# Kernel optimization log

Measured on AMD Instinct MI355X. Metric: run time of the kernel, lower is better.

The kernel has to match this reference:

```python
import jax, jax.numpy as jnp
import numpy as np
import math

P = 2
TAU = 1.0
USE_POW = False
ALIGN_W = 1.0
ENTROPY_W = 1.0
EPS = 1e-12


def _pairwise_l2(z):
    # torch.cdist(z, z, p=2): sqrt of squared distances via GEMM decomposition
    sq = jnp.sum(z * z, axis=-1)  # [N]
    d2 = sq[:, None] + sq[None, :] - 2.0 * (z @ z.T)  # [N, N]
    d = jnp.sqrt(jnp.maximum(d2, 0.0))
    return jnp.maximum(d, EPS)  # clamp_min(eps)


def setup_inputs() -> dict:
    key = jax.random.key(0)
    k0, k1 = jax.random.split(key)
    v0 = jax.random.normal(k0, (8192, 256), dtype=jnp.float32)
    v1 = jax.random.normal(k1, (8192, 256), dtype=jnp.float32)
    return {"v0": v0, "v1": v1}


def reference(v0, v1):
    views = [v0, v1]
    n = v0.shape[0]

    # Alignment term: mean Lp distance between matched rows, one pair (0,1)
    diff = v0 - v1
    align = jnp.sqrt(jnp.sum(diff * diff, axis=-1)).mean()  # p=2 norm per row

    # Entropy term: masked logsumexp over within-view pairwise distances
    log_num_neg = math.log(n - 1)
    eye = jnp.eye(n, dtype=bool)
    entropy = jnp.float32(0.0)
    for z in views:
        dist = _pairwise_l2(z)  # [N, N]
        logits = jnp.where(eye, -jnp.inf, -dist / TAU)
        lme = jax.nn.logsumexp(logits, axis=1) - log_num_neg  # [N]
        entropy = entropy + lme.mean()
    entropy = entropy / len(views)

    return ALIGN_W * align + ENTROPY_W * entropy
```

## Files before the change

### kernel.cpp

```cpp
#include <hip/hip_runtime.h>
#include <math.h>


#define D_DIM 256
#define NB 64
#define NSEG 1056
#define S_Q 26.0f
#define LOG2E2 2.0813689810f
#define LP 65

typedef int i32x4 __attribute__((ext_vector_type(4)));
typedef unsigned int u32;
#define AS1 __attribute__((address_space(1)))
#define AS3 __attribute__((address_space(3)))

__device__ inline void load_lds16(const void* g, void* l) {
  __builtin_amdgcn_global_load_lds((const AS1 u32*)g, (AS3 u32*)l, 16, 0, 0);
}

__device__ inline int q8(float x) {
  return __float2int_rn(fminf(fmaxf(x * S_Q, -127.0f), 127.0f));
}
__device__ inline u32 q8x4(const float4 f) {
  return (u32)(q8(f.x) & 255) | ((u32)(q8(f.y) & 255) << 8) |
         ((u32)(q8(f.z) & 255) << 16) | ((u32)(q8(f.w) & 255) << 24);
}

__device__ inline int Gfun(int M) {
  const int m = M >> 1;
  return (M & 1) ? (m + 1) * (m + 1) : m * (m + 1);
}

__global__ __launch_bounds__(256) void prep(
    const float* __restrict__ v0, const float* __restrict__ v1,
    unsigned char* __restrict__ ph0, unsigned char* __restrict__ ph1,
    float* __restrict__ sq0, float* __restrict__ sq1,
    float* __restrict__ S0, float* __restrict__ S1,
    float* __restrict__ align_part) {
  __shared__ float4 l0[16 * LP], l1[16 * LP];
  __shared__ float red0[4][16], red1[4][16], red2[4][16];
  const int R = blockIdx.x;
  const int t = threadIdx.x;

  #pragma unroll
  for (int p = 0; p < 4; ++p) {
    const int slot = t + p * 256;
    const int r = slot >> 6, col = slot & 63;
    const size_t g = (size_t)(R * 16 + r) * 64 + col;
    l0[r * LP + col] = ((const float4*)v0)[g];
    l1[r * LP + col] = ((const float4*)v1)[g];
  }
  __syncthreads();

  {
    const int rr = t & 15, c = t >> 4;
    const int s = c >> 2, q = c & 3;
    const int li = rr * LP + c * 4;
    uint4 u0, u1;
    u0.x = q8x4(l0[li + 0]); u0.y = q8x4(l0[li + 1]);
    u0.z = q8x4(l0[li + 2]); u0.w = q8x4(l0[li + 3]);
    u1.x = q8x4(l1[li + 0]); u1.y = q8x4(l1[li + 1]);
    u1.z = q8x4(l1[li + 2]); u1.w = q8x4(l1[li + 3]);
    const size_t dst = (size_t)(R * 4 + s) * 64 + q * 16 + rr;
    ((uint4*)ph0)[dst] = u0;
    ((uint4*)ph1)[dst] = u1;
  }

  {
    const int rr = t & 15;
    const int base = rr * LP + (t >> 4) * 4;
    float s0p = 0.f, s1p = 0.f, s2p = 0.f;
    #pragma unroll
    for (int c = 0; c < 4; ++c) {
      const float4 a = l0[base + c], b = l1[base + c];
      s0p += a.x * a.x + a.y * a.y + a.z * a.z + a.w * a.w;
      s1p += b.x * b.x + b.y * b.y + b.z * b.z + b.w * b.w;
      const float dx = a.x - b.x, dy = a.y - b.y, dz = a.z - b.z, dw = a.w - b.w;
      s2p += dx * dx + dy * dy + dz * dz + dw * dw;
    }
    s0p += __shfl_xor(s0p, 16, 64); s0p += __shfl_xor(s0p, 32, 64);
    s1p += __shfl_xor(s1p, 16, 64); s1p += __shfl_xor(s1p, 32, 64);
    s2p += __shfl_xor(s2p, 16, 64); s2p += __shfl_xor(s2p, 32, 64);
    const int w = t >> 6, lane = t & 63;
    if (lane < 16) { red0[w][lane] = s0p; red1[w][lane] = s1p; red2[w][lane] = s2p; }
  }
  __syncthreads();
  if (t < 16) {
    const int row = R * 16 + t;
    const float a0 = red0[0][t] + red0[1][t] + red0[2][t] + red0[3][t];
    const float a1 = red1[0][t] + red1[1][t] + red1[2][t] + red1[3][t];
    const float a2 = red2[0][t] + red2[1][t] + red2[2][t] + red2[3][t];
    sq0[row] = a0 * LOG2E2;
    sq1[row] = a1 * LOG2E2;
    align_part[row] = sqrtf(a2);
    S0[row] = 0.0f;
    S1[row] = 0.0f;
  }
}

__global__ __launch_bounds__(256) void entropy_tile(
    const unsigned char* __restrict__ ph0, const unsigned char* __restrict__ ph1,
    const float* __restrict__ sq0, const float* __restrict__ sq1,
    float* __restrict__ S0, float* __restrict__ S1) {
  const unsigned char* __restrict__ ph = blockIdx.y ? ph1 : ph0;
  const float* __restrict__ sq = blockIdx.y ? sq1 : sq0;
  float* __restrict__ S        = blockIdx.y ? S1 : S0;

  const int lin = blockIdx.x;
  int bi = 0;
  while (NSEG - Gfun(64 - (bi + 1)) <= lin) ++bi;
  const int q = lin - (NSEG - Gfun(64 - bi));
  const int bj0 = bi + 2 * q;

  __shared__ __align__(16) char smem[32768];
  float* swp = (float*)smem;

  const int t = threadIdx.x, lane = t & 63, w = t >> 6;
  const int wi = w >> 1, wj = w & 1;
  const int quad = lane >> 4, l15 = lane & 15;
  const int i0 = bi * 128;

  #pragma unroll
  for (int r8 = 0; r8 < 8; ++r8) {
    const int seg = w * 8 + r8;
    const unsigned char* src = ph + (size_t)bi * 32768 + seg * 1024 + lane * 16;
    load_lds16(src, smem + seg * 1024);
  }
  __syncthreads();

  const i32x4* __restrict__ phv = (const i32x4*)ph;
  const i32x4* smemv = (const i32x4*)smem;
  const float K2 = 2.0f * LOG2E2 / (S_Q * S_Q);

  float prow[4][4];
  #pragma unroll
  for (int m = 0; m < 4; ++m)
    #pragma unroll
    for (int r = 0; r < 4; ++r) prow[m][r] = 0.f;

  auto do_tile = [&](const int bj, const bool diag_t) {
    const int j0 = bj * 128;
    const int baseB = ((bj * 8 + wj * 4) * 4) * 64 + lane;

    float sjl[4];
    #pragma unroll
    for (int n = 0; n < 4; ++n) sjl[n] = sq[j0 + wj * 64 + n * 16 + l15];

    i32x4 bF[4][4];
    #pragma unroll
    for (int s = 0; s < 4; ++s)
      #pragma unroll
      for (int n = 0; n < 4; ++n)
        bF[s][n] = phv[baseB + (n * 4 + s) * 64];

    float csum[4] = {0.f, 0.f, 0.f, 0.f};

    i32x4 accA[4], accB[4];
    float siA[4], siB[4];

    auto compute = [&](i32x4* acc, float* si, const int m) {
      #pragma unroll
      for (int r = 0; r < 4; ++r)
        si[r] = sq[i0 + wi * 64 + m * 16 + quad * 4 + r];
      #pragma unroll
      for (int n = 0; n < 4; ++n) acc[n] = (i32x4){0, 0, 0, 0};
      #pragma unroll
      for (int s = 0; s < 4; ++s) {
        const i32x4 ah = smemv[(size_t)((wi * 4 + m) * 4 + s) * 64 + lane];
        #pragma unroll
        for (int n = 0; n < 4; ++n)
          acc[n] = __builtin_amdgcn_mfma_i32_16x16x64_i8(ah, bF[s][n], acc[n], 0, 0, 0);
      }
    };

    auto epilogue = [&](const i32x4* acc, const float* si, const int m) {
      #pragma unroll
      for (int r = 0; r < 4; ++r) {
        const int gi = i0 + wi * 64 + m * 16 + quad * 4 + r;
        float p = 0.f;
        #pragma unroll
        for (int n = 0; n < 4; ++n) {
          const float d2 = fmaf(-K2, (float)acc[n][r], si[r] + sjl[n]);
          float e = __builtin_amdgcn_exp2f(-__builtin_amdgcn_sqrtf(d2));
          if (diag_t && gi == j0 + wj * 64 + n * 16 + l15) e = 0.f;
          p += e;
          csum[n] += e;
        }
        prow[m][r] += p;
      }
    };

    compute(accA, siA, 0);
    compute(accB, siB, 1);
    epilogue(accA, siA, 0);
    compute(accA, siA, 2);
    epilogue(accB, siB, 1);
    compute(accB, siB, 3);
    epilogue(accA, siA, 2);
    epilogue(accB, siB, 3);

    if (!diag_t) {
      #pragma unroll
      for (int n = 0; n < 4; ++n) {
        float c2 = csum[n];
        c2 += __shfl_xor(c2, 16, 64);
        c2 += __shfl_xor(c2, 32, 64);
        if (quad == 0) atomicAdd(&S[j0 + wj * 64 + n * 16 + l15], c2);
      }
    }
  };

  if (bj0 == bi) do_tile(bi, true); else do_tile(bj0, false);
  if (bj0 + 1 < NB) do_tile(bj0 + 1, false);

  __syncthreads();

  const int wbase = w * 1088;
  #pragma unroll
  for (int m = 0; m < 4; ++m)
    #pragma unroll
    for (int r = 0; r < 4; ++r)
      swp[wbase + (m * 16 + quad * 4 + r) * 17 + l15] = prow[m][r];
  float rs = 0.f;
  #pragma unroll
  for (int j = 0; j < 16; ++j) rs += swp[wbase + lane * 17 + j];
  atomicAdd(&S[i0 + wi * 64 + lane], rs);
}

__global__ __launch_bounds__(256) void finalize_part(
    const float* __restrict__ S0, const float* __restrict__ S1,
    const float* __restrict__ align_part,
    float* __restrict__ part_log, float* __restrict__ part_align) {
  __shared__ float shl[4], sha[4];
  const int t = threadIdx.x, lane = t & 63, w = t >> 6;
  const int idx = blockIdx.x * 256 + t;
  float lg = __logf(S0[idx]) + __logf(S1[idx]);
  float al = align_part[idx];
  #pragma unroll
  for (int o = 1; o < 64; o <<= 1) {
    lg += __shfl_xor(lg, o, 64);
    al += __shfl_xor(al, o, 64);
  }
  if (lane == 0) { shl[w] = lg; sha[w] = al; }
  __syncthreads();
  if (t == 0) {
    part_log[blockIdx.x] = shl[0] + shl[1] + shl[2] + shl[3];
    part_align[blockIdx.x] = sha[0] + sha[1] + sha[2] + sha[3];
  }
}

__global__ void finalize_final(const float* __restrict__ part_log,
                               const float* __restrict__ part_align,
                               float* __restrict__ out, int n) {
  const int lane = threadIdx.x & 63;
  double lg = (lane < 32) ? (double)part_log[lane] : 0.0;
  double al = (lane < 32) ? (double)part_align[lane] : 0.0;
  #pragma unroll
  for (int o = 1; o < 32; o <<= 1) {
    lg += __shfl_xor(lg, o, 64);
    al += __shfl_xor(al, o, 64);
  }
  if (lane == 0) {
    double align = al / (double)n;
    double entropy = 0.5 * lg / (double)n - log((double)(n - 1));
    out[0] = (float)(align + entropy);
  }
}

extern "C" void kernel_launch(void* const* d_in, const int* in_sizes, int n_in,
                              void* d_out, int out_size, void* d_ws, size_t ws_size,
                              hipStream_t stream) {
  const float* v0 = (const float*)d_in[0];
  const float* v1 = (const float*)d_in[1];
  float* out = (float*)d_out;
  const int n = in_sizes[0] / D_DIM;

  float* ws         = (float*)d_ws;
  float* sq0        = ws;
  float* sq1        = ws + n;
  float* S0         = ws + 2 * n;
  float* S1         = ws + 3 * n;
  float* align_part = ws + 4 * n;
  float* part_log   = ws + 5 * n;
  float* part_align = ws + 5 * n + 32;
  unsigned char* ph0 = (unsigned char*)(ws + 5 * n + 64);
  unsigned char* ph1 = ph0 + (size_t)n * D_DIM;

  prep<<<n / 16, 256, 0, stream>>>(v0, v1, ph0, ph1, sq0, sq1, S0, S1, align_part);

  dim3 grid(NSEG, 2);
  entropy_tile<<<grid, 256, 0, stream>>>(ph0, ph1, sq0, sq1, S0, S1);

  finalize_part<<<n / 256, 256, 0, stream>>>(S0, S1, align_part, part_log, part_align);
  finalize_final<<<1, 64, 0, stream>>>(part_log, part_align, out, n);
}
```

Baseline: 112.7 us.

## Prefetch next B tile during epilogue and fuse final reduction via atomic ticket

The entropy tile kernel now issues the global loads for the second column tile's B fragments and squared norms before the epilogue of the first tile runs, so their latency overlaps with exp/sqrt work. The first tile's B loads are also issued before the barrier that waits on the LDS fill. Separately, the two finalize kernels are merged into one, which accumulates partial sums with double atomics and lets the last block, chosen by an atomic ticket, write the output. This saves a kernel launch, but the accumulation order becomes nondeterministic and the prefetch keeps more registers live.

```diff
diff --git a/kernel.cpp b/kernel.cpp
--- a/kernel.cpp
+++ b/kernel.cpp
@@ -36,11 +36,14 @@
     unsigned char* __restrict__ ph0, unsigned char* __restrict__ ph1,
     float* __restrict__ sq0, float* __restrict__ sq1,
     float* __restrict__ S0, float* __restrict__ S1,
-    float* __restrict__ align_part) {
+    float* __restrict__ align_part,
+    double* __restrict__ totals, int* __restrict__ ticket) {
   __shared__ float4 l0[16 * LP], l1[16 * LP];
   __shared__ float red0[4][16], red1[4][16], red2[4][16];
   const int R = blockIdx.x;
   const int t = threadIdx.x;
+
+  if (R == 0 && t == 0) { totals[0] = 0.0; totals[1] = 0.0; ticket[0] = 0; }
 
   #pragma unroll
   for (int p = 0; p < 4; ++p) {
@@ -126,92 +129,112 @@
     const unsigned char* src = ph + (size_t)bi * 32768 + seg * 1024 + lane * 16;
     load_lds16(src, smem + seg * 1024);
   }
-  __syncthreads();
 
   const i32x4* __restrict__ phv = (const i32x4*)ph;
   const i32x4* smemv = (const i32x4*)smem;
   const float K2 = 2.0f * LOG2E2 / (S_Q * S_Q);
 
+  const int bjA = bj0;
+  const bool diagA = (bj0 == bi);
+  const bool haveB = (bj0 + 1 < NB);
+  const int j0A = bjA * 128;
+
   float prow[4][4];
   #pragma unroll
   for (int m = 0; m < 4; ++m)
     #pragma unroll
     for (int r = 0; r < 4; ++r) prow[m][r] = 0.f;
 
-  auto do_tile = [&](const int bj, const bool diag_t) {
-    const int j0 = bj * 128;
+  i32x4 bF[4][4];
+  float sjlA[4], sjlB[4];
+  float csumA[4] = {0.f, 0.f, 0.f, 0.f}, csumB[4] = {0.f, 0.f, 0.f, 0.f};
+  i32x4 accA[4], accB[4];
+  float siA[4], siB[4];
+
+  auto loadB = [&](const int bj) {
     const int baseB = ((bj * 8 + wj * 4) * 4) * 64 + lane;
-
-    float sjl[4];
-    #pragma unroll
-    for (int n = 0; n < 4; ++n) sjl[n] = sq[j0 + wj * 64 + n * 16 + l15];
-
-    i32x4 bF[4][4];
     #pragma unroll
     for (int s = 0; s < 4; ++s)
       #pragma unroll
       for (int n = 0; n < 4; ++n)
         bF[s][n] = phv[baseB + (n * 4 + s) * 64];
-
-    float csum[4] = {0.f, 0.f, 0.f, 0.f};
-
-    i32x4 accA[4], accB[4];
-    float siA[4], siB[4];
-
-    auto compute = [&](i32x4* acc, float* si, const int m) {
+  };
+  auto loadSj = [&](const int bj, float* sjl) {
+    #pragma unroll
+    for (int n = 0; n < 4; ++n) sjl[n] = sq[bj * 128 + wj * 64 + n * 16 + l15];
+  };
+
+  loadSj(bjA, sjlA);
+  loadB(bjA);
+  __syncthreads();
+
+  auto compute = [&](i32x4* acc, float* si, const int m) {
+    #pragma unroll
+    for (int r = 0; r < 4; ++r)
+      si[r] = sq[i0 + wi * 64 + m * 16 + quad * 4 + r];
+    #pragma unroll
+    for (int n = 0; n < 4; ++n) acc[n] = (i32x4){0, 0, 0, 0};
+    #pragma unroll
+    for (int s = 0; s < 4; ++s) {
+      const i32x4 ah = smemv[(size_t)((wi * 4 + m) * 4 + s) * 64 + lane];
       #pragma unroll
-      for (int r = 0; r < 4; ++r)
-        si[r] = sq[i0 + wi * 64 + m * 16 + quad * 4 + r];
+      for (int n = 0; n < 4; ++n)
+        acc[n] = __builtin_amdgcn_mfma_i32_16x16x64_i8(ah, bF[s][n], acc[n], 0, 0, 0);
+    }
+  };
+
+  auto epilogue = [&](const i32x4* acc, const float* si, const int m,
+                      const float* sjl, float* csum, const int j0,
+                      const bool diag_t) {
+    #pragma unroll
+    for (int r = 0; r < 4; ++r) {
+      const int gi = i0 + wi * 64 + m * 16 + quad * 4 + r;
+      float p = 0.f;
       #pragma unroll
-      for (int n = 0; n < 4; ++n) acc[n] = (i32x4){0, 0, 0, 0};
-      #pragma unroll
-      for (int s = 0; s < 4; ++s) {
-        const i32x4 ah = smemv[(size_t)((wi * 4 + m) * 4 + s) * 64 + lane];
-        #pragma unroll
-        for (int n = 0; n < 4; ++n)
-          acc[n] = __builtin_amdgcn_mfma_i32_16x16x64_i8(ah, bF[s][n], acc[n], 0, 0, 0);
+      for (int n = 0; n < 4; ++n) {
+        const float d2 = fmaf(-K2, (float)acc[n][r], si[r] + sjl[n]);
+        float e = __builtin_amdgcn_exp2f(-__builtin_amdgcn_sqrtf(d2));
+        if (diag_t && gi == j0 + wj * 64 + n * 16 + l15) e = 0.f;
+        p += e;
+        csum[n] += e;
       }
-    };
-
-    auto epilogue = [&](const i32x4* acc, const float* si, const int m) {
-      #pragma unroll
-      for (int r = 0; r < 4; ++r) {
-        const int gi = i0 + wi * 64 + m * 16 + quad * 4 + r;
-        float p = 0.f;
-        #pragma unroll
-        for (int n = 0; n < 4; ++n) {
-          const float d2 = fmaf(-K2, (float)acc[n][r], si[r] + sjl[n]);
-          float e = __builtin_amdgcn_exp2f(-__builtin_amdgcn_sqrtf(d2));
-          if (diag_t && gi == j0 + wj * 64 + n * 16 + l15) e = 0.f;
-          p += e;
-          csum[n] += e;
-        }
-        prow[m][r] += p;
-      }
-    };
-
+      prow[m][r] += p;
+    }
+  };
+
+  auto flushCsum = [&](const float* csum, const int j0) {
+    #pragma unroll
+    for (int n = 0; n < 4; ++n) {
+      float c2 = csum[n];
+      c2 += __shfl_xor(c2, 16, 64);
+      c2 += __shfl_xor(c2, 32, 64);
+      if (quad == 0) atomicAdd(&S[j0 + wj * 64 + n * 16 + l15], c2);
+    }
+  };
+
+  compute(accA, siA, 0);
+  compute(accB, siB, 1);
+  epilogue(accA, siA, 0, sjlA, csumA, j0A, diagA);
+  compute(accA, siA, 2);
+  epilogue(accB, siB, 1, sjlA, csumA, j0A, diagA);
+  compute(accB, siB, 3);
+  if (haveB) { loadSj(bjA + 1, sjlB); loadB(bjA + 1); }
+  epilogue(accA, siA, 2, sjlA, csumA, j0A, diagA);
+  epilogue(accB, siB, 3, sjlA, csumA, j0A, diagA);
+  if (!diagA) flushCsum(csumA, j0A);
+
+  if (haveB) {
+    const int j0B = (bjA + 1) * 128;
     compute(accA, siA, 0);
     compute(accB, siB, 1);
-    epilogue(accA, siA, 0);
+    epilogue(accA, siA, 0, sjlB, csumB, j0B, false);
     compute(accA, siA, 2);
-    epilogue(accB, siB, 1);
+    epilogue(accB, siB, 1, sjlB, csumB, j0B, false);
     compute(accB, siB, 3);
-    epilogue(accA, siA, 2);
-    epilogue(accB, siB, 3);
-
-    if (!diag_t) {
-      #pragma unroll
-      for (int n = 0; n < 4; ++n) {
-        float c2 = csum[n];
-        c2 += __shfl_xor(c2, 16, 64);
-        c2 += __shfl_xor(c2, 32, 64);
-        if (quad == 0) atomicAdd(&S[j0 + wj * 64 + n * 16 + l15], c2);
-      }
-    }
-  };
-
-  if (bj0 == bi) do_tile(bi, true); else do_tile(bj0, false);
-  if (bj0 + 1 < NB) do_tile(bj0 + 1, false);
+    epilogue(accA, siA, 2, sjlB, csumB, j0B, false);
+    epilogue(accB, siB, 3, sjlB, csumB, j0B, false);
+    flushCsum(csumB, j0B);
+  }
 
   __syncthreads();
 
@@ -227,10 +250,11 @@
   atomicAdd(&S[i0 + wi * 64 + lane], rs);
 }
 
-__global__ __launch_bounds__(256) void finalize_part(
+__global__ __launch_bounds__(256) void finalize_fused(
     const float* __restrict__ S0, const float* __restrict__ S1,
     const float* __restrict__ align_part,
-    float* __restrict__ part_log, float* __restrict__ part_align) {
+    double* __restrict__ totals, int* __restrict__ ticket,
+    float* __restrict__ out, int n) {
   __shared__ float shl[4], sha[4];
   const int t = threadIdx.x, lane = t & 63, w = t >> 6;
   const int idx = blockIdx.x * 256 + t;
@@ -244,26 +268,19 @@
   if (lane == 0) { shl[w] = lg; sha[w] = al; }
   __syncthreads();
   if (t == 0) {
-    part_log[blockIdx.x] = shl[0] + shl[1] + shl[2] + shl[3];
-    part_align[blockIdx.x] = sha[0] + sha[1] + sha[2] + sha[3];
-  }
-}
-
-__global__ void finalize_final(const float* __restrict__ part_log,
-                               const float* __restrict__ part_align,
-                               float* __restrict__ out, int n) {
-  const int lane = threadIdx.x & 63;
-  double lg = (lane < 32) ? (double)part_log[lane] : 0.0;
-  double al = (lane < 32) ? (double)part_align[lane] : 0.0;
-  #pragma unroll
-  for (int o = 1; o < 32; o <<= 1) {
-    lg += __shfl_xor(lg, o, 64);
-    al += __shfl_xor(al, o, 64);
-  }
-  if (lane == 0) {
-    double align = al / (double)n;
-    double entropy = 0.5 * lg / (double)n - log((double)(n - 1));
-    out[0] = (float)(align + entropy);
+    const double pl = (double)(shl[0] + shl[1] + shl[2] + shl[3]);
+    const double pa = (double)(sha[0] + sha[1] + sha[2] + sha[3]);
+    atomicAdd(&totals[0], pl);
+    atomicAdd(&totals[1], pa);
+    __threadfence();
+    const int old = atomicAdd(ticket, 1);
+    if (old == (int)gridDim.x - 1) {
+      const double lgt = atomicAdd(&totals[0], 0.0);
+      const double alt = atomicAdd(&totals[1], 0.0);
+      const double align = alt / (double)n;
+      const double entropy = 0.5 * lgt / (double)n - log((double)(n - 1));
+      out[0] = (float)(align + entropy);
+    }
   }
 }
 
@@ -281,16 +298,17 @@
   float* S0         = ws + 2 * n;
   float* S1         = ws + 3 * n;
   float* align_part = ws + 4 * n;
-  float* part_log   = ws + 5 * n;
-  float* part_align = ws + 5 * n + 32;
+  double* totals    = (double*)(ws + 5 * n);
+  int* ticket       = (int*)(ws + 5 * n + 4);
   unsigned char* ph0 = (unsigned char*)(ws + 5 * n + 64);
   unsigned char* ph1 = ph0 + (size_t)n * D_DIM;
 
-  prep<<<n / 16, 256, 0, stream>>>(v0, v1, ph0, ph1, sq0, sq1, S0, S1, align_part);
+  prep<<<n / 16, 256, 0, stream>>>(v0, v1, ph0, ph1, sq0, sq1, S0, S1,
+                                   align_part, totals, ticket);
 
   dim3 grid(NSEG, 2);
   entropy_tile<<<grid, 256, 0, stream>>>(ph0, ph1, sq0, sq1, S0, S1);
 
-  finalize_part<<<n / 256, 256, 0, stream>>>(S0, S1, align_part, part_log, part_align);
-  finalize_final<<<1, 64, 0, stream>>>(part_log, part_align, out, n);
-}
+  finalize_fused<<<n / 256, 256, 0, stream>>>(S0, S1, align_part, totals,
+                                              ticket, out, n);
+}
```

After: 134.8 us. +19.6%, slower.
